# Kernel optimization log

Measured on AMD Instinct MI355X. Metric: run time of the kernel, lower is better.

The kernel has to match this reference:

```python
import jax, jax.numpy as jnp
import numpy as np
from math import factorial

# ----- hyperparams (mirror init_kwargs) -----
HIDDEN = [(32,0,1),(32,0,-1),(8,1,1),(8,1,-1),(4,2,1),(4,2,-1)]  # (mul, l, parity)
SCALAR = [(32,0,1)]
SH_IRR = [(1,0,1),(1,1,-1),(1,2,1)]  # spherical harmonics 0e+1o+2e
EMB, NUM_RBF, R_MAX, MLP_DIM, D_IN = 32, 16, 10.0, 256, 64
N_NODES, N_EDGES, N_GRAPHS = 2048, 8192, 8
EDGE_FEATS_DIM = NUM_RBF + 2*EMB

def _slices(irs):
    s, o = [], 0
    for m, l, _ in irs:
        s.append(o); o += m*(2*l+1)
    return s

def _su2_cg(j1, j2, j3, m1, m2, m3):
    if m1 + m2 != m3:
        return 0.0
    f = factorial
    pref = ((2*j3+1)*f(j3+j1-j2)*f(j3-j1+j2)*f(j1+j2-j3)/f(j1+j2+j3+1))**0.5
    pref *= (f(j3+m3)*f(j3-m3)*f(j1-m1)*f(j1+m1)*f(j2-m2)*f(j2+m2))**0.5
    s = 0.0
    for k in range(0, j1+j2-j3+1):
        if j1-m1-k < 0 or j2+m2-k < 0 or j3-j2+m1+k < 0 or j3-j1-m2+k < 0:
            continue
        s += (-1.0)**k/(f(k)*f(j1+j2-j3-k)*f(j1-m1-k)*f(j2+m2-k)*f(j3-j2+m1+k)*f(j3-j1-m2+k))
    return pref*s

def _q(l):  # real -> complex change of basis (e3nn convention incl. (-i)^l phase)
    q = np.zeros((2*l+1, 2*l+1), dtype=np.complex128)
    for m in range(-l, 0):
        q[l+m, l+abs(m)] = 2**-0.5
        q[l+m, l-abs(m)] = -1j*2**-0.5
    q[l, l] = 1.0
    for m in range(1, l+1):
        q[l+m, l+abs(m)] = (-1)**m*2**-0.5
        q[l+m, l-abs(m)] = 1j*(-1)**m*2**-0.5
    return (-1j)**l*q

def _real_cg(l1, l2, l3):  # real-basis Clebsch-Gordan, unit Frobenius norm (wigner-3j-like)
    C = np.zeros((2*l1+1, 2*l2+1, 2*l3+1), dtype=np.complex128)
    for m1 in range(-l1, l1+1):
        for m2 in range(-l2, l2+1):
            m3 = m1 + m2
            if abs(m3) <= l3:
                C[l1+m1, l2+m2, l3+m3] = _su2_cg(l1, l2, l3, m1, m2, m3)
    w = np.einsum('ai,bj,ck,abc->ijk', _q(l1), _q(l2), np.conj(_q(l3)), C)
    re, im = np.real(w), np.imag(w)
    w = re if np.linalg.norm(re) >= np.linalg.norm(im) else im
    return (w/np.linalg.norm(w)).astype(np.float32)

_CG = {}
def cg(l1, l2, l3):
    if (l1, l2, l3) not in _CG:
        _CG[(l1, l2, l3)] = jnp.asarray(_real_cg(l1, l2, l3))
    return _CG[(l1, l2, l3)]

def _build_layer(ir_in, ir_out):  # FullyConnectedTensorProduct path enumeration
    si = _slices(ir_in)
    paths, woff, fan = [], 0, [0]*len(ir_out)
    for i1, (m1, l1, p1) in enumerate(ir_in):
        for (_, l2, p2) in SH_IRR:
            for i3, (m3, l3, p3) in enumerate(ir_out):
                if p1*p2 == p3 and abs(l1-l2) <= l3 <= l1+l2:
                    paths.append((si[i1], m1, l1, l2, i3, m3, l3, woff))
                    fan[i3] += m1
                    woff += m1*m3
    return paths, woff, fan, ir_out

L_SPECS = [_build_layer(SCALAR, HIDDEN), _build_layer(HIDDEN, HIDDEN),
           _build_layer(HIDDEN, HIDDEN), _build_layer(HIDDEN, SCALAR)]
W_NUMELS = [s[1] for s in L_SPECS]  # [1408, 4320, 4320, 1408]

def spherical_harmonics(u):  # component-normalized real SH, l=0,1,2, on unit vectors
    xc, yc, zc = u[:, 0], u[:, 1], u[:, 2]
    s3, s15, s5 = 3**0.5, 15**0.5, 5**0.5
    return jnp.stack([jnp.ones_like(xc),
                      s3*yc, s3*zc, s3*xc,
                      s15*xc*yc, s15*yc*zc, s5*0.5*(3*zc*zc-1.0), s15*xc*zc,
                      s15*0.5*(xc*xc-yc*yc)], axis=1)

def tp_messages(x, sh, w, spec):  # per-edge equivariant tensor product with edge-dep weights
    paths, _, fan, ir_out = spec
    E = x.shape[0]
    outs = [jnp.zeros((E, m*(2*l+1)), x.dtype) for m, l, _ in ir_out]
    for (o1, m1, l1, l2, i3, m3, l3, woff) in paths:
        xp = x[:, o1:o1+m1*(2*l1+1)].reshape(E, m1, 2*l1+1)
        shp = sh[:, l2*l2:(l2+1)*(l2+1)]
        wp = w[:, woff:woff+m1*m3].reshape(E, m1, m3)
        alpha = float(np.sqrt((2*l3+1)/fan[i3]))  # component/element path normalization
        y = alpha*jnp.einsum('eui,ej,euv,ijk->evk', xp, shp, wp, cg(l1, l2, l3))
        outs[i3] = outs[i3] + y.reshape(E, -1)
    return jnp.concatenate(outs, axis=1)

def batch_norm(h, ir_out, eps=1e-5):  # e3nn-style equivariant batch norm (train stats, identity affine)
    outs, o = [], 0
    for m, l, _ in ir_out:
        d = m*(2*l+1)
        f = h[:, o:o+d].reshape(-1, m, 2*l+1); o += d
        if l == 0:
            f = f - f.mean(axis=0, keepdims=True)
        norm2 = (f*f).mean(axis=(0, 2), keepdims=True)
        outs.append((f*jax.lax.rsqrt(norm2+eps)).reshape(h.shape[0], -1))
    return jnp.concatenate(outs, axis=1)

def scatter_mean(msg, idx, n):
    s = jax.ops.segment_sum(msg, idx, num_segments=n)
    c = jax.ops.segment_sum(jnp.ones((idx.shape[0], 1), msg.dtype), idx, num_segments=n)
    return s/jnp.maximum(c, 1.0)

def _forward(x, pos, edge_index, batch, emb_w, emb_b, layer_params):
    ei = jnp.concatenate([edge_index, edge_index[::-1]], axis=1)  # to_undirected (both directions)
    src, dst = ei[0], ei[1]
    h = x@emb_w + emb_b  # (N, 32)
    vec = pos[src] - pos[dst]
    lengths = jnp.linalg.norm(vec, axis=-1)
    sh = spherical_harmonics(vec/lengths[:, None])  # (E, 9)
    mu = jnp.linspace(0.0, R_MAX, NUM_RBF)
    sigma = R_MAX/NUM_RBF
    rbf = jnp.exp(-(((lengths[:, None]-mu)/sigma)**2))  # (E, 16)
    for li, (w1, b1, w2, b2) in enumerate(layer_params):
        ef = jnp.concatenate([rbf, h[src, :EMB], h[dst, :EMB]], axis=1)  # (E, 80)
        w = jax.nn.relu(ef@w1 + b1)@w2 + b2  # per-edge TP weights (dropout=eval noop)
        upd = scatter_mean(tp_messages(h[dst], sh, w, L_SPECS[li]), src, N_NODES)
        upd = batch_norm(upd, L_SPECS[li][3])
        d = upd.shape[-1]
        h_res = h[:, :d] if h.shape[-1] >= d else jnp.pad(h, ((0, 0), (0, d-h.shape[-1])))
        h = upd + h_res  # residual with pad/truncate (F.pad semantics)
    graph = jax.ops.segment_sum(h, batch, num_segments=N_GRAPHS)
    return h, graph

def setup_inputs():
    key = jax.random.key(0)
    ks = jax.random.split(key, 32)
    inp = {}
    inp['x'] = jax.random.normal(ks[0], (N_NODES, D_IN), jnp.float32)
    inp['pos'] = 3.0*jax.random.normal(ks[1], (N_NODES, 3), jnp.float32)
    s = jax.random.randint(ks[2], (N_EDGES,), 0, N_NODES)
    d = (s + jax.random.randint(ks[3], (N_EDGES,), 1, N_NODES)) % N_NODES  # no self-loops
    inp['edge_index'] = jnp.stack([s, d]).astype(jnp.int32)
    inp['batch'] = jnp.sort(jax.random.randint(ks[4], (N_NODES,), 0, N_GRAPHS)).astype(jnp.int32)
    inp['emb_w'] = jax.random.normal(ks[5], (D_IN, EMB), jnp.float32)/np.sqrt(D_IN)
    inp['emb_b'] = jnp.zeros((EMB,), jnp.float32)
    k = 6
    for i, wn in enumerate(W_NUMELS):
        inp[f'l{i}_w1'] = jax.random.normal(ks[k], (EDGE_FEATS_DIM, MLP_DIM), jnp.float32)/np.sqrt(EDGE_FEATS_DIM); k += 1
        inp[f'l{i}_b1'] = jnp.zeros((MLP_DIM,), jnp.float32)
        inp[f'l{i}_w2'] = jax.random.normal(ks[k], (MLP_DIM, wn), jnp.float32)/np.sqrt(MLP_DIM); k += 1
        inp[f'l{i}_b2'] = jnp.zeros((wn,), jnp.float32)
    return inp

def reference(x, pos, edge_index, batch, emb_w, emb_b,
              l0_w1, l0_b1, l0_w2, l0_b2, l1_w1, l1_b1, l1_w2, l1_b2,
              l2_w1, l2_b1, l2_w2, l2_b2, l3_w1, l3_b1, l3_w2, l3_b2):
    lp = [(l0_w1, l0_b1, l0_w2, l0_b2), (l1_w1, l1_b1, l1_w2, l1_b2),
          (l2_w1, l2_b1, l2_w2, l2_b2), (l3_w1, l3_b1, l3_w2, l3_b2)]
    return _forward(x, pos, edge_index, batch, emb_w, emb_b, lp)
```

## Files before the change

### kernel.cpp

```cpp
#include <hip/hip_runtime.h>
#include <hip/hip_bf16.h>
#include <math.h>

#define NNODES 2048
#define NEDG   8192
#define E2     16384
#define NGRAPH 8
#define HSTR   152

static const int LD_DIN[4]  = {32,152,152,152};
static const int LD_DOUT[4] = {152,152,152,32};
static const int LD_WN[4]   = {1408,4320,4320,1408};
static const int LD_WNP[4]  = {1408,4352,4352,1408};
static const int LD_NCH[4]  = {88,88,88,32};
static const int LD_RES[4]  = {32,152,152,152};
#define WNP_MAX 4352

#define SLOT_MAX    1088
#define CELL_N      20
#define SEG_S_N     164
#define SEG_ENT_MAX 1024

typedef short bf16x8 __attribute__((ext_vector_type(8)));
typedef float f32x4  __attribute__((ext_vector_type(4)));

constexpr double cfact(int n){ double r=1.0; for(int i=2;i<=n;i++) r*=(double)i; return r; }
constexpr double csqrt(double x){
  if(x<=0.0) return 0.0;
  double g = x>1.0? x:1.0;
  for(int i=0;i<64;i++) g=0.5*(g+x/g);
  return g;
}
constexpr double csu2cg(int j1,int j2,int j3,int m1,int m2,int m3){
  if(m1+m2!=m3) return 0.0;
  double pref = csqrt((double)(2*j3+1)*cfact(j3+j1-j2)*cfact(j3-j1+j2)*cfact(j1+j2-j3)/cfact(j1+j2+j3+1));
  pref *= csqrt(cfact(j3+m3)*cfact(j3-m3)*cfact(j1-m1)*cfact(j1+m1)*cfact(j2-m2)*cfact(j2+m2));
  double s=0.0;
  for(int k=0;k<=j1+j2-j3;k++){
    if(j1-m1-k<0||j2+m2-k<0||j3-j2+m1+k<0||j3-j1-m2+k<0) continue;
    double t=1.0/(cfact(k)*cfact(j1+j2-j3-k)*cfact(j1-m1-k)*cfact(j2+m2-k)*cfact(j3-j2+m1+k)*cfact(j3-j1-m2+k));
    s += (k&1)? -t : t;
  }
  return pref*s;
}
struct QM { double r[25]; double i[25]; };
constexpr QM cqmat(int l){
  QM q{};
  const double inv2=0.7071067811865476;
  for(int m=-l;m<0;m++){
    int am=-m;
    q.r[(l+m)*5+(l+am)] = inv2;
    q.i[(l+m)*5+(l-am)] = -inv2;
  }
  q.r[l*5+l]=1.0;
  for(int m=1;m<=l;m++){
    double sgn=(m&1)? -1.0:1.0;
    q.r[(l+m)*5+(l+m)] = sgn*inv2;
    q.i[(l+m)*5+(l-m)] = sgn*inv2;
  }
  for(int rep=0;rep<l;rep++){
    for(int t=0;t<25;t++){ double a=q.r[t], b=q.i[t]; q.r[t]=b; q.i[t]=-a; }
  }
  return q;
}
struct CGCell { float v[125]; };
constexpr CGCell mkcell(int l1,int l2,int l3){
  CGCell out{};
  int lo = l1>l2? l1-l2 : l2-l1;
  if(l3<lo || l3>l1+l2) return out;
  QM q1=cqmat(l1), q2=cqmat(l2), q3=cqmat(l3);
  int n1=2*l1+1,n2=2*l2+1,n3=2*l3+1;
  double C[125]={};
  for(int a=0;a<n1;a++)for(int b=0;b<n2;b++)for(int c=0;c<n3;c++)
    C[a*25+b*5+c]=csu2cg(l1,l2,l3,a-l1,b-l2,c-l3);
  double wr[125]={}, wi[125]={};
  for(int i=0;i<n1;i++)for(int j=0;j<n2;j++)for(int k=0;k<n3;k++){
    double ar=0.0, ai=0.0;
    for(int a=0;a<n1;a++)for(int b=0;b<n2;b++){
      double p1r=q1.r[a*5+i], p1i=q1.i[a*5+i];
      double p2r=q2.r[b*5+j], p2i=q2.i[b*5+j];
      double pr=p1r*p2r-p1i*p2i, pi=p1r*p2i+p1i*p2r;
      for(int c=0;c<n3;c++){
        double cv=C[a*25+b*5+c]; if(cv==0.0) continue;
        double p3r=q3.r[c*5+k], p3i=-q3.i[c*5+k];
        ar += (pr*p3r-pi*p3i)*cv;
        ai += (pr*p3i+pi*p3r)*cv;
      }
    }
    wr[i*25+j*5+k]=ar; wi[i*25+j*5+k]=ai;
  }
  double sr=0.0, si=0.0;
  for(int t=0;t<125;t++){ sr+=wr[t]*wr[t]; si+=wi[t]*wi[t]; }
  double nr=csqrt(sr), ni=csqrt(si);
  bool use_re = nr>=ni;
  double nn = use_re? nr:ni;
  double inv = (nn>1e-300)? 1.0/nn : 0.0;
  for(int t=0;t<125;t++) out.v[t]=(float)((use_re? wr[t]:wi[t])*inv);
  return out;
}
constexpr CGCell CGc0 =mkcell(0,0,0), CGc1 =mkcell(0,0,1), CGc2 =mkcell(0,0,2);
constexpr CGCell CGc3 =mkcell(0,1,0), CGc4 =mkcell(0,1,1), CGc5 =mkcell(0,1,2);
constexpr CGCell CGc6 =mkcell(0,2,0), CGc7 =mkcell(0,2,1), CGc8 =mkcell(0,2,2);
constexpr CGCell CGc9 =mkcell(1,0,0), CGc10=mkcell(1,0,1), CGc11=mkcell(1,0,2);
constexpr CGCell CGc12=mkcell(1,1,0), CGc13=mkcell(1,1,1), CGc14=mkcell(1,1,2);
constexpr CGCell CGc15=mkcell(1,2,0), CGc16=mkcell(1,2,1), CGc17=mkcell(1,2,2);
constexpr CGCell CGc18=mkcell(2,0,0), CGc19=mkcell(2,0,1), CGc20=mkcell(2,0,2);
constexpr CGCell CGc21=mkcell(2,1,0), CGc22=mkcell(2,1,1), CGc23=mkcell(2,1,2);
constexpr CGCell CGc24=mkcell(2,2,0), CGc25=mkcell(2,2,1), CGc26=mkcell(2,2,2);
__constant__ CGCell g_cg[27] = {
  CGc0,CGc1,CGc2,CGc3,CGc4,CGc5,CGc6,CGc7,CGc8,
  CGc9,CGc10,CGc11,CGc12,CGc13,CGc14,CGc15,CGc16,CGc17,
  CGc18,CGc19,CGc20,CGc21,CGc22,CGc23,CGc24,CGc25,CGc26};

#define MAXP 32
struct LayerSpec {
  int np, zc, wn, nc;
  int x_off[MAXP], m1[MAXP], d1[MAXP], sh_off[MAXP], d2[MAXP], d3[MAXP],
      m3[MAXP], woff[MAXP], out_sl[MAXP], cg_idx[MAXP], zbase[MAXP], cell[MAXP];
  float alpha[MAXP];
  int cellcg[16];
};
constexpr LayerSpec mkspec(int li){
  LayerSpec S{};
  const int IRH[6][3]={{32,0,1},{32,0,-1},{8,1,1},{8,1,-1},{4,2,1},{4,2,-1}};
  const int IRS[1][3]={{32,0,1}};
  const int SH2[3][2]={{0,1},{1,-1},{2,1}};
  const int (*irin)[3]  = (li==0)? IRS: IRH; int nin =(li==0)?1:6;
  const int (*irout)[3] = (li==3)? IRS: IRH; int nout=(li==3)?1:6;
  int si_in[6]={}, si_out[6]={};
  { int o=0; for(int i=0;i<nin;i++){ si_in[i]=o;  o+=irin[i][0]*(2*irin[i][1]+1);} }
  { int o=0; for(int i=0;i<nout;i++){ si_out[i]=o; o+=irout[i][0]*(2*irout[i][1]+1);} }
  int fan[6]={};
  int i3a[MAXP]={};
  int np=0, woff=0, zb=0, nc=0;
  for(int i1=0;i1<nin;i1++){
    int m1=irin[i1][0], l1=irin[i1][1], p1=irin[i1][2];
    for(int s=0;s<3;s++){
      int l2=SH2[s][0], p2=SH2[s][1];
      for(int i3=0;i3<nout;i3++){
        int m3=irout[i3][0], l3=irout[i3][1], p3=irout[i3][2];
        int lo = l1>l2? l1-l2 : l2-l1;
        if(p1*p2==p3 && l3>=lo && l3<=l1+l2){
          S.x_off[np]=si_in[i1]; S.m1[np]=m1; S.d1[np]=2*l1+1;
          S.sh_off[np]=l2*l2; S.d2[np]=2*l2+1; S.d3[np]=2*l3+1;
          S.m3[np]=m3; S.woff[np]=woff; S.out_sl[np]=si_out[i3];
          S.cg_idx[np]=l1*9+l2*3+l3; S.zbase[np]=zb;
          int ci=-1;
          for(int c=0;c<nc;c++) if(S.cellcg[c]==S.cg_idx[np]) ci=c;
          if(ci<0){ S.cellcg[nc]=S.cg_idx[np]; ci=nc++; }
          S.cell[np]=ci; i3a[np]=i3;
          np++;
          fan[i3]+=m1; woff+=m1*m3; zb+=m1*(2*l3+1);
        }
      }
    }
  }
  for(int p=0;p<np;p++)
    S.alpha[p]=(float)csqrt((double)(2*((S.d3[p]-1)/2)+1)/(double)fan[i3a[p]]);
  S.np=np; S.zc=zb; S.wn=woff; S.nc=nc;
  return S;
}
constexpr LayerSpec LS0=mkspec(0), LS1=mkspec(1), LS2=mkspec(2), LS3=mkspec(3);
__constant__ LayerSpec g_spec[4]={LS0,LS1,LS2,LS3};

__global__ __launch_bounds__(256) void build_tables_kernel(
    unsigned* __restrict__ slot_tab, unsigned* __restrict__ cell_tab,
    int* __restrict__ seg_start, unsigned* __restrict__ seg_ent,
    int* __restrict__ perm, float* __restrict__ alpha_col){
  __shared__ int vals[256];
  __shared__ int part[256];
  int tid=threadIdx.x;
  int li=blockIdx.x;
  const LayerSpec& S=g_spec[li];
  int np=S.np, zc=S.zc, nc=S.nc, wn=S.wn;
  for(int c=tid;c<nc;c+=256){
    int cgi=S.cellcg[c];
    int l2=(cgi/3)%3;
    cell_tab[li*CELL_N+c]=(unsigned)cgi | ((unsigned)(l2*l2)<<8) | ((unsigned)(2*l2+1)<<12);
  }
  for(int s=tid;s<zc;s+=256){
    int p=0; while(p+1<np && S.zbase[p+1]<=s) p++;
    int rel=s-S.zbase[p];
    int k=rel/S.m1[p], u=rel-k*S.m1[p];
    slot_tab[li*SLOT_MAX+s]=(unsigned)(S.x_off[p]+u*S.d1[p]) | ((unsigned)k<<9) | ((unsigned)S.cell[p]<<12);
  }
  int* pm=perm+li*WNP_MAX;
  float* ac=alpha_col+li*WNP_MAX;
  for(int j=tid;j<wn;j+=256){
    int p=0; while(p+1<np && S.woff[p+1]<=j) p++;
    int rel=j-S.woff[p];
    int v=rel/S.m1[p], u=rel%S.m1[p];
    pm[j]=S.woff[p]+u*S.m3[p]+v;
    ac[j]=S.alpha[p];
  }
  int Dout=(li==3)?32:152;
  for(int d=tid;d<Dout;d+=256){
    int cnt=0;
    for(int p=0;p<np;p++){
      int rel=d-S.out_sl[p];
      if(rel>=0 && rel<S.m3[p]*S.d3[p]) cnt++;
    }
    vals[d]=cnt;
  }
  __syncthreads();
  int v0=(tid<Dout)? vals[tid]:0;
  part[tid]=v0;
  __syncthreads();
  for(int ofs=1;ofs<256;ofs<<=1){
    int v=(tid>=ofs)? part[tid-ofs]:0;
    __syncthreads();
    part[tid]+=v;
    __syncthreads();
  }
  int* sst=seg_start+li*SEG_S_N;
  if(tid<Dout) sst[tid]=part[tid]-v0;
  if(tid==0) sst[Dout]=part[255];
  __syncthreads();
  unsigned* se=seg_ent+li*SEG_ENT_MAX;
  for(int d=tid;d<Dout;d+=256){
    int pos=sst[d];
    for(int p=0;p<np;p++){
      int rel=d-S.out_sl[p];
      if(rel>=0 && rel<S.m3[p]*S.d3[p]){
        int v=rel/S.d3[p], k=rel%S.d3[p];
        unsigned z0=(unsigned)(S.zbase[p]+k*S.m1[p]);
        unsigned w0=(unsigned)(S.woff[p]+v*S.m1[p]);
        unsigned code=(S.m1[p]==32)?2u:((S.m1[p]==8)?1u:0u);
        se[pos]= z0 | (w0<<11) | (code<<24);
        pos++;
      }
    }
  }
}

__global__ void geom_kernel(const float* __restrict__ pos, const int* __restrict__ ei,
                            int* __restrict__ src2, int* __restrict__ dst2,
                            float* __restrict__ sh, float* __restrict__ rbf,
                            int* __restrict__ counts){
  int e=blockIdx.x*256+threadIdx.x;
  if(e>=E2) return;
  int s,d;
  if(e<NEDG){ s=ei[e]; d=ei[NEDG+e]; }
  else { int j=e-NEDG; s=ei[NEDG+j]; d=ei[j]; }
  src2[e]=s; dst2[e]=d;
  atomicAdd(&counts[s],1);
  float vx=pos[s*3+0]-pos[d*3+0];
  float vy=pos[s*3+1]-pos[d*3+1];
  float vz=pos[s*3+2]-pos[d*3+2];
  float len=sqrtf(vx*vx+vy*vy+vz*vz);
  float inv=1.f/len;
  float x=vx*inv, y=vy*inv, z=vz*inv;
  const float s3=1.7320508075688772f, s15=3.872983346207417f, s5=2.23606797749979f;
  float* shp=sh+(size_t)e*9;
  shp[0]=1.f; shp[1]=s3*y; shp[2]=s3*z; shp[3]=s3*x;
  shp[4]=s15*x*y; shp[5]=s15*y*z; shp[6]=s5*0.5f*(3.f*z*z-1.f);
  shp[7]=s15*x*z; shp[8]=s15*0.5f*(x*x-y*y);
  float* rp=rbf+(size_t)e*16;
  const float invsig=1.6f;
  for(int k=0;k<16;k++){
    float t=(len-(10.0f/15.0f)*(float)k)*invsig;
    rp[k]=expf(-t*t);
  }
}

__global__ void scan_kernel(const int* __restrict__ counts, int* __restrict__ row_ptr){
  __shared__ int part[256];
  int t=threadIdx.x;
  int base=t*8;
  int loc[8]; int s=0;
  #pragma unroll
  for(int i=0;i<8;i++){ loc[i]=counts[base+i]; s+=loc[i]; }
  part[t]=s; __syncthreads();
  for(int ofs=1; ofs<256; ofs<<=1){
    int v=(t>=ofs)? part[t-ofs]:0;
    __syncthreads();
    part[t]+=v;
    __syncthreads();
  }
  int run=part[t]-s;
  #pragma unroll
  for(int i=0;i<8;i++){ row_ptr[base+i]=run; run+=loc[i]; }
  if(t==255) row_ptr[NNODES]=run;
}

__global__ void csr_fill_kernel(const int* __restrict__ src2, const int* __restrict__ row_ptr,
                                int* __restrict__ cursor, int* __restrict__ eidx){
  int e=blockIdx.x*256+threadIdx.x;
  if(e>=E2) return;
  int s=src2[e];
  int p=atomicAdd(&cursor[s],1);
  eidx[row_ptr[s]+p]=e;
}

__global__ void embed_kernel(const float* __restrict__ x, const float* __restrict__ W,
                             const float* __restrict__ b, float* __restrict__ h){
  int idx=blockIdx.x*256+threadIdx.x;
  int n=idx>>5, j=idx&31;
  float acc=b[j];
  for(int k=0;k<64;k++) acc += x[n*64+k]*W[k*32+j];
  h[(size_t)n*HSTR+j]=acc;
}

__global__ void cast_w2t_kernel(const float* __restrict__ w2, const int* __restrict__ perm,
                                const float* __restrict__ alpha_col,
                                __hip_bfloat16* __restrict__ w2t, int wn, int wn_pad){
  int idx=blockIdx.x*256+threadIdx.x;
  if(idx>=wn_pad*256) return;
  int j=idx>>8, k=idx&255;
  float v=(j<wn)? w2[(size_t)k*wn+perm[j]]*alpha_col[j] : 0.f;
  w2t[idx]=__float2bfloat16(v);
}

__global__ __launch_bounds__(256) void mlp1_kernel(
    const float* __restrict__ h, const float* __restrict__ rbf,
    const int* __restrict__ src2, const int* __restrict__ dst2,
    const float* __restrict__ w1, const float* __restrict__ b1,
    __hip_bfloat16* __restrict__ hidden, int e_start){
  __shared__ float ef[16][80];
  int tid=threadIdx.x;
  int e0=e_start+blockIdx.x*16;
  for(int t=tid;t<16*80;t+=256){
    int el=t/80, k=t-el*80; int ge=e0+el;
    float v;
    if(k<16)      v=rbf[(size_t)ge*16+k];
    else if(k<48) v=h[(size_t)src2[ge]*HSTR+(k-16)];
    else          v=h[(size_t)dst2[ge]*HSTR+(k-48)];
    ef[el][k]=v;
  }
  __syncthreads();
  float acc[16];
  float bv=b1[tid];
  #pragma unroll
  for(int e=0;e<16;e++) acc[e]=bv;
  for(int k=0;k<80;k++){
    float wv=w1[k*256+tid];
    #pragma unroll
    for(int e=0;e<16;e++) acc[e]+=ef[e][k]*wv;
  }
  int le0=blockIdx.x*16;
  #pragma unroll
  for(int e=0;e<16;e++)
    hidden[(size_t)(le0+e)*256+tid]=__float2bfloat16(fmaxf(acc[e],0.f));
}

__global__ __launch_bounds__(256) void mlp2_mfma_kernel(
    const __hip_bfloat16* __restrict__ hidden,
    const __hip_bfloat16* __restrict__ w2t,
    const float* __restrict__ b2, const int* __restrict__ perm,
    const float* __restrict__ alpha_col,
    __hip_bfloat16* __restrict__ wbuf, int wn, int wn_pad){
  __shared__ __hip_bfloat16 As[128*32];
  __shared__ __hip_bfloat16 Bs[128*32];
  int tid=threadIdx.x;
  int lane=tid&63;
  int m0=blockIdx.x*128, n0=blockIdx.y*128;
  int mw=((tid>>6)&1)*64, nw=(tid>>7)*64;
  f32x4 acc[4][4];
  #pragma unroll
  for(int i=0;i<4;i++)
    #pragma unroll
    for(int j=0;j<4;j++) acc[i][j]=(f32x4){0.f,0.f,0.f,0.f};

  int i0=tid*8, i1=tid*8+2048;
  int ar0=i0>>5, ac0=i0&31, ar1=i1>>5, ac1=i1&31;
  const int q4=lane>>4, c16=lane&15;

  for(int k0=0;k0<256;k0+=32){
    __syncthreads();
    *(uint4*)&As[ar0*32+ac0] = *(const uint4*)&hidden[(size_t)(m0+ar0)*256 + k0 + ac0];
    *(uint4*)&As[ar1*32+ac1] = *(const uint4*)&hidden[(size_t)(m0+ar1)*256 + k0 + ac1];
    *(uint4*)&Bs[ar0*32+ac0] = *(const uint4*)&w2t[(size_t)(n0+ar0)*256 + k0 + ac0];
    *(uint4*)&Bs[ar1*32+ac1] = *(const uint4*)&w2t[(size_t)(n0+ar1)*256 + k0 + ac1];
    __syncthreads();
    bf16x8 af[4], bfr[4];
    #pragma unroll
    for(int mi=0;mi<4;mi++) af[mi]=*(bf16x8*)&As[(mw+mi*16+c16)*32 + q4*8];
    #pragma unroll
    for(int ni=0;ni<4;ni++) bfr[ni]=*(bf16x8*)&Bs[(nw+ni*16+c16)*32 + q4*8];
    #pragma unroll
    for(int mi=0;mi<4;mi++)
      #pragma unroll
      for(int ni=0;ni<4;ni++)
        acc[mi][ni]=__builtin_amdgcn_mfma_f32_16x16x32_bf16(af[mi],bfr[ni],acc[mi][ni],0,0,0);
  }
  #pragma unroll
  for(int ni=0;ni<4;ni++){
    int col=n0+nw+ni*16+c16;
    float bias=(col<wn)? b2[perm[col]]*alpha_col[col]:0.f;
    #pragma unroll
    for(int mi=0;mi<4;mi++){
      int row=m0+mw+mi*16+q4*4;
      #pragma unroll
      for(int rr=0;rr<4;rr++)
        wbuf[(size_t)(row+rr)*wn_pad+col]=__float2bfloat16(acc[mi][ni][rr]+bias);
    }
  }
}

__device__ inline void wave_sync(){
  __builtin_amdgcn_s_waitcnt(0);
  __builtin_amdgcn_wave_barrier();
}

__device__ inline float dot8l(const float* zp, const __hip_bfloat16* wp){
  f32x4 za=*(const f32x4*)zp;
  f32x4 zb=*(const f32x4*)(zp+4);
  uint4 wv=*(const uint4*)wp;
  const __hip_bfloat16* wl=(const __hip_bfloat16*)&wv;
  float s=0.f;
  #pragma unroll
  for(int t=0;t<4;t++) s+=za[t]*__bfloat162float(wl[t]);
  #pragma unroll
  for(int t=0;t<4;t++) s+=zb[t]*__bfloat162float(wl[4+t]);
  return s;
}
__device__ inline float dot4l(const float* zp, const __hip_bfloat16* wp){
  f32x4 za=*(const f32x4*)zp;
  uint2 wv=*(const uint2*)wp;
  const __hip_bfloat16* wl=(const __hip_bfloat16*)&wv;
  float s=0.f;
  #pragma unroll
  for(int t=0;t<4;t++) s+=za[t]*__bfloat162float(wl[t]);
  return s;
}

__global__ __launch_bounds__(128) void tp5_kernel(
    const float* __restrict__ h, const float* __restrict__ sh,
    const __hip_bfloat16* __restrict__ wbuf, const int* __restrict__ dst2,
    const unsigned* __restrict__ slot_tab, const unsigned* __restrict__ cell_tab,
    const int* __restrict__ seg_start, const unsigned* __restrict__ seg_ent,
    float* __restrict__ msg, int e_start, int Din, int Dout, int wstride,
    int zc, int nc){
  __shared__ float xrow[2][160];
  __shared__ float shs[2][12];
  __shared__ float zsm[2][1088];
  __shared__ float Tw[2][376];
  __shared__ __hip_bfloat16 wlds[2][WNP_MAX];
  int tid=threadIdx.x, w=tid>>6, lane=tid&63;
  int le=blockIdx.x*2+w, ge=e_start+le;
  int dn=dst2[ge];
  const __hip_bfloat16* wrow=wbuf+(size_t)le*wstride;
  for(int t=lane;t<(wstride>>3);t+=64)
    *(uint4*)&wlds[w][t*8] = *(const uint4*)&wrow[(size_t)t*8];
  for(int i=lane;i<Din;i+=64) xrow[w][i]=h[(size_t)dn*HSTR+i];
  for(int i=Din+lane;i<160;i+=64) xrow[w][i]=0.f;
  if(lane<9) shs[w][lane]=sh[(size_t)ge*9+lane];
  wave_sync();
  float* T=&Tw[w][0];
  for(int t=lane;t<nc*25;t+=64){
    int c=t/25, r=t-c*25, k=r/5, i=r-k*5;
    unsigned cm=cell_tab[c];
    int cgi=cm&255, sho=(cm>>8)&15, d2=(cm>>12)&7;
    const float* cgp=g_cg[cgi].v + i*25 + k;
    float s=0.f;
    for(int j=0;j<d2;j++) s+=cgp[j*5]*shs[w][sho+j];
    T[t]=s;
  }
  wave_sync();
  const float* xr=&xrow[w][0];
  for(int s=lane;s<zc;s+=64){
    unsigned st=slot_tab[s];
    int xb=st&511, k=(st>>9)&7, c=st>>12;
    const float* Tp=&T[c*25+k*5];
    zsm[w][s]=xr[xb]*Tp[0]+xr[xb+1]*Tp[1]+xr[xb+2]*Tp[2]+xr[xb+3]*Tp[3]+xr[xb+4]*Tp[4];
  }
  wave_sync();
  const __hip_bfloat16* wl=&wlds[w][0];
  const float* zbase=&zsm[w][0];
  for(int d=lane;d<Dout;d+=64){
    int s0=seg_start[d], s1=seg_start[d+1];
    float acc=0.f;
    for(int s=s0;s<s1;s++){
      unsigned sg=seg_ent[s];
      int z0=sg&2047, w0=(sg>>11)&8191, code=sg>>24;
      const float* zp=zbase+z0;
      const __hip_bfloat16* wp=wl+w0;
      if(code==2){
        #pragma unroll
        for(int t=0;t<4;t++) acc+=dot8l(zp+t*8,wp+t*8);
      } else if(code==1){
        acc+=dot8l(zp,wp);
      } else {
        acc+=dot4l(zp,wp);
      }
    }
    msg[(size_t)ge*Dout+d]=acc;
  }
}

__global__ void aggregate_kernel(const float* __restrict__ msg, const int* __restrict__ row_ptr,
                                 const int* __restrict__ eidx, const int* __restrict__ counts,
                                 float* __restrict__ upd, int Dout){
  int n=blockIdx.x; int lane=threadIdx.x;
  int p0=row_ptr[n], p1=row_ptr[n+1];
  int c=counts[n]; if(c<1) c=1;
  float inv=1.f/(float)c;
  for(int d=lane;d<Dout;d+=64){
    float s=0.f;
    for(int p=p0;p<p1;p++) s+=msg[(size_t)eidx[p]*Dout+d];
    upd[(size_t)n*Dout+d]=s*inv;
  }
}

__device__ inline int hidden_chan_of_dim(int d){
  if(d<64)  return d;
  if(d<88)  return 64+(d-64)/3;
  if(d<112) return 72+(d-88)/3;
  if(d<132) return 80+(d-112)/5;
  return 84+(d-132)/5;
}
__device__ inline void hidden_chan_params(int c, int& off, int& dk, int& l0){
  if(c<64){ off=c; dk=1; l0=1; }
  else if(c<72){ off=64+(c-64)*3; dk=3; l0=0; }
  else if(c<80){ off=88+(c-72)*3; dk=3; l0=0; }
  else if(c<84){ off=112+(c-80)*5; dk=5; l0=0; }
  else { off=132+(c-84)*5; dk=5; l0=0; }
}

__global__ void stats_kernel(const float* __restrict__ upd, float* __restrict__ stats,
                             int Dout, int scalar_out){
  int c=blockIdx.x, tid=threadIdx.x;
  int off,dk,l0;
  if(scalar_out){ off=c; dk=1; l0=1; }
  else hidden_chan_params(c,off,dk,l0);
  float s=0.f, s2=0.f;
  int total=NNODES*dk;
  for(int t=tid;t<total;t+=256){
    int n=t/dk, k=t-n*dk;
    float v=upd[(size_t)n*Dout+off+k];
    s+=v; s2+=v*v;
  }
  __shared__ float rs[256], rs2[256];
  rs[tid]=s; rs2[tid]=s2; __syncthreads();
  for(int o=128;o>0;o>>=1){
    if(tid<o){ rs[tid]+=rs[tid+o]; rs2[tid]+=rs2[tid+o]; }
    __syncthreads();
  }
  if(tid==0){
    float cnt=(float)total;
    float mean = l0? rs[0]/cnt : 0.f;
    float var = rs2[0]/cnt - mean*mean;
    stats[c*2]=mean;
    stats[c*2+1]=1.0f/sqrtf(var+1e-5f);
  }
}

__global__ void apply_kernel(const float* __restrict__ upd, const float* __restrict__ stats,
                             const float* __restrict__ h_cur, float* __restrict__ h_next,
                             int Dout, int res_dim, int scalar_out, int out_stride){
  int idx=blockIdx.x*256+threadIdx.x;
  if(idx>=NNODES*Dout) return;
  int n=idx/Dout, d=idx-n*Dout;
  int c = scalar_out? d : hidden_chan_of_dim(d);
  float v=(upd[idx]-stats[2*c])*stats[2*c+1];
  float res=(d<res_dim)? h_cur[(size_t)n*HSTR+d] : 0.f;
  h_next[(size_t)n*out_stride+d]=v+res;
}

__global__ void graph_kernel(const float* __restrict__ hfin, const int* __restrict__ batch,
                             float* __restrict__ gout){
  int idx=blockIdx.x*256+threadIdx.x;
  int n=idx>>5, d=idx&31;
  atomicAdd(&gout[batch[n]*32+d], hfin[idx]);
}

extern "C" void kernel_launch(void* const* d_in, const int* in_sizes, int n_in,
                              void* d_out, int out_size, void* d_ws, size_t ws_size,
                              hipStream_t stream){
  (void)in_sizes; (void)n_in; (void)out_size;
  const float* x    =(const float*)d_in[0];
  const float* pos  =(const float*)d_in[1];
  const int*   ei   =(const int*)d_in[2];
  const int*   batch=(const int*)d_in[3];
  const float* emb_w=(const float*)d_in[4];
  const float* emb_b=(const float*)d_in[5];
  const float *W1[4], *B1[4], *W2[4], *B2[4];
  for(int l=0;l<4;l++){
    W1[l]=(const float*)d_in[6+4*l];
    B1[l]=(const float*)d_in[7+4*l];
    W2[l]=(const float*)d_in[8+4*l];
    B2[l]=(const float*)d_in[9+4*l];
  }
  int ZC[4]={LS0.zc,LS1.zc,LS2.zc,LS3.zc};
  int NC[4]={LS0.nc,LS1.nc,LS2.nc,LS3.nc};

  char* base=(char*)d_ws;
  size_t off=0;
  auto alloc=[&](size_t bytes)->char*{
    off=(off+255)&~(size_t)255;
    char* p=base+off; off+=bytes; return p;
  };
  float*  h_a   =(float*)alloc((size_t)NNODES*HSTR*4);
  float*  h_b   =(float*)alloc((size_t)NNODES*HSTR*4);
  float*  shb   =(float*)alloc((size_t)E2*9*4);
  float*  rbfb  =(float*)alloc((size_t)E2*16*4);
  int*    src2  =(int*)  alloc((size_t)E2*4);
  int*    dst2  =(int*)  alloc((size_t)E2*4);
  int*    counts=(int*)  alloc((size_t)NNODES*4);
  int*    cursor=(int*)  alloc((size_t)NNODES*4);
  int*    row_ptr=(int*) alloc((size_t)(NNODES+4)*4);
  int*    eidx  =(int*)  alloc((size_t)E2*4);
  float*  msg   =(float*)alloc((size_t)E2*HSTR*4);
  float*  upd   =(float*)alloc((size_t)NNODES*HSTR*4);
  float*  stats =(float*)alloc(256*4);
  unsigned* slot_tab=(unsigned*)alloc((size_t)4*SLOT_MAX*4);
  unsigned* cell_tg =(unsigned*)alloc((size_t)4*CELL_N*4);
  int*      seg_s   =(int*)     alloc((size_t)4*SEG_S_N*4);
  unsigned* seg_e   =(unsigned*)alloc((size_t)4*SEG_ENT_MAX*4);
  int*      perm    =(int*)     alloc((size_t)4*WNP_MAX*4);
  float*    alpha_c =(float*)   alloc((size_t)4*WNP_MAX*4);
  __hip_bfloat16* w2t[4];
  for(int l=0;l<4;l++) w2t[l]=(__hip_bfloat16*)alloc((size_t)LD_WNP[l]*256*2);

  int E_CHUNK=E2;
  while(E_CHUNK>128){
    size_t need=off;
    need=(need+255)&~(size_t)255; need+=(size_t)E_CHUNK*256*2;
    need=(need+255)&~(size_t)255; need+=(size_t)E_CHUNK*WNP_MAX*2;
    if(need<=ws_size) break;
    E_CHUNK>>=1;
  }
  __hip_bfloat16* hidden=(__hip_bfloat16*)alloc((size_t)E_CHUNK*256*2);
  __hip_bfloat16* wbuf  =(__hip_bfloat16*)alloc((size_t)E_CHUNK*WNP_MAX*2);

  hipMemsetAsync(counts,0,(size_t)NNODES*4,stream);
  hipMemsetAsync(cursor,0,(size_t)NNODES*4,stream);
  build_tables_kernel<<<4,256,0,stream>>>(slot_tab,cell_tg,seg_s,seg_e,perm,alpha_c);
  geom_kernel<<<E2/256,256,0,stream>>>(pos,ei,src2,dst2,shb,rbfb,counts);
  scan_kernel<<<1,256,0,stream>>>(counts,row_ptr);
  csr_fill_kernel<<<E2/256,256,0,stream>>>(src2,row_ptr,cursor,eidx);
  embed_kernel<<<(NNODES*32)/256,256,0,stream>>>(x,emb_w,emb_b,h_a);
  for(int l=0;l<4;l++)
    cast_w2t_kernel<<<(LD_WNP[l]*256+255)/256,256,0,stream>>>(
        W2[l],perm+l*WNP_MAX,alpha_c+l*WNP_MAX,w2t[l],LD_WN[l],LD_WNP[l]);

  float* h_cur=h_a; float* h_nxt=h_b;
  for(int li=0;li<4;li++){
    int wn=LD_WN[li], wnp=LD_WNP[li], Din=LD_DIN[li], Dout=LD_DOUT[li];
    for(int e0=0;e0<E2;e0+=E_CHUNK){
      mlp1_kernel<<<E_CHUNK/16,256,0,stream>>>(h_cur,rbfb,src2,dst2,W1[li],B1[li],hidden,e0);
      dim3 g2(E_CHUNK/128, wnp/128);
      mlp2_mfma_kernel<<<g2,256,0,stream>>>(hidden,w2t[li],B2[li],perm+li*WNP_MAX,
                                            alpha_c+li*WNP_MAX,wbuf,wn,wnp);
      tp5_kernel<<<E_CHUNK/2,128,0,stream>>>(h_cur,shb,wbuf,dst2,
          slot_tab+li*SLOT_MAX, cell_tg+li*CELL_N,
          seg_s+li*SEG_S_N, seg_e+li*SEG_ENT_MAX,
          msg,e0,Din,Dout,wnp, ZC[li], NC[li]);
    }
    aggregate_kernel<<<NNODES,64,0,stream>>>(msg,row_ptr,eidx,counts,upd,Dout);
    stats_kernel<<<LD_NCH[li],256,0,stream>>>(upd,stats,Dout,li==3?1:0);
    int tot=NNODES*Dout;
    if(li<3)
      apply_kernel<<<(tot+255)/256,256,0,stream>>>(upd,stats,h_cur,h_nxt,Dout,LD_RES[li],0,HSTR);
    else
      apply_kernel<<<(tot+255)/256,256,0,stream>>>(upd,stats,h_cur,(float*)d_out,Dout,LD_RES[li],1,32);
    float* tmp=h_cur; h_cur=h_nxt; h_nxt=tmp;
  }

  float* gout=(float*)d_out + (size_t)NNODES*32;
  hipMemsetAsync(gout,0,(size_t)NGRAPH*32*4,stream);
  graph_kernel<<<(NNODES*32)/256,256,0,stream>>>((const float*)d_out,batch,gout);
}
```

Before: 895.3 us.

## Read per-edge TP weights directly from global memory and interleave output segments

The tensor-product kernel no longer stages each edge's weight row into LDS and instead reads bf16 weights straight from global memory inside the segment dot products. It also packs four edges per 256-thread block instead of two, and each lane now handles up to three output channels in one interleaved loop rather than a strided outer loop. The aim is to cut LDS footprint, raising occupancy, and to remove the staging copy and its barrier. The cost is uncoalesced, scattered global loads of weights, and extra predicated work when the three channels have different segment counts.

```diff
diff --git a/kernel.cpp b/kernel.cpp
--- a/kernel.cpp
+++ b/kernel.cpp
@@ -402,46 +402,56 @@
   __builtin_amdgcn_wave_barrier();
 }
 
-__device__ inline float dot8l(const float* zp, const __hip_bfloat16* wp){
-  f32x4 za=*(const f32x4*)zp;
-  f32x4 zb=*(const f32x4*)(zp+4);
-  uint4 wv=*(const uint4*)wp;
-  const __hip_bfloat16* wl=(const __hip_bfloat16*)&wv;
+__device__ inline float seg_dot(unsigned sg, const float* zbase, const __hip_bfloat16* wrow){
+  int z0=sg&2047, w0=(sg>>11)&8191, code=sg>>24;
+  const float* zp=zbase+z0;
+  const __hip_bfloat16* wp=wrow+w0;
   float s=0.f;
-  #pragma unroll
-  for(int t=0;t<4;t++) s+=za[t]*__bfloat162float(wl[t]);
-  #pragma unroll
-  for(int t=0;t<4;t++) s+=zb[t]*__bfloat162float(wl[4+t]);
+  if(code==2){
+    #pragma unroll
+    for(int t=0;t<4;t++){
+      f32x4 za=*(const f32x4*)(zp+t*8);
+      f32x4 zb=*(const f32x4*)(zp+t*8+4);
+      uint4 wv=*(const uint4*)(wp+t*8);
+      const __hip_bfloat16* wl=(const __hip_bfloat16*)&wv;
+      #pragma unroll
+      for(int q=0;q<4;q++) s+=za[q]*__bfloat162float(wl[q]);
+      #pragma unroll
+      for(int q=0;q<4;q++) s+=zb[q]*__bfloat162float(wl[4+q]);
+    }
+  } else if(code==1){
+    f32x4 za=*(const f32x4*)zp;
+    f32x4 zb=*(const f32x4*)(zp+4);
+    uint4 wv=*(const uint4*)wp;
+    const __hip_bfloat16* wl=(const __hip_bfloat16*)&wv;
+    #pragma unroll
+    for(int q=0;q<4;q++) s+=za[q]*__bfloat162float(wl[q]);
+    #pragma unroll
+    for(int q=0;q<4;q++) s+=zb[q]*__bfloat162float(wl[4+q]);
+  } else {
+    f32x4 za=*(const f32x4*)zp;
+    uint2 wv=*(const uint2*)wp;
+    const __hip_bfloat16* wl=(const __hip_bfloat16*)&wv;
+    #pragma unroll
+    for(int q=0;q<4;q++) s+=za[q]*__bfloat162float(wl[q]);
+  }
   return s;
 }
-__device__ inline float dot4l(const float* zp, const __hip_bfloat16* wp){
-  f32x4 za=*(const f32x4*)zp;
-  uint2 wv=*(const uint2*)wp;
-  const __hip_bfloat16* wl=(const __hip_bfloat16*)&wv;
-  float s=0.f;
-  #pragma unroll
-  for(int t=0;t<4;t++) s+=za[t]*__bfloat162float(wl[t]);
-  return s;
-}
-
-__global__ __launch_bounds__(128) void tp5_kernel(
+
+__global__ __launch_bounds__(256) void tp6_kernel(
     const float* __restrict__ h, const float* __restrict__ sh,
     const __hip_bfloat16* __restrict__ wbuf, const int* __restrict__ dst2,
     const unsigned* __restrict__ slot_tab, const unsigned* __restrict__ cell_tab,
     const int* __restrict__ seg_start, const unsigned* __restrict__ seg_ent,
     float* __restrict__ msg, int e_start, int Din, int Dout, int wstride,
     int zc, int nc){
-  __shared__ float xrow[2][160];
-  __shared__ float shs[2][12];
-  __shared__ float zsm[2][1088];
-  __shared__ float Tw[2][376];
-  __shared__ __hip_bfloat16 wlds[2][WNP_MAX];
+  __shared__ float xrow[4][160];
+  __shared__ float shs[4][12];
+  __shared__ float zsm[4][1088];
+  __shared__ float Tw[4][376];
   int tid=threadIdx.x, w=tid>>6, lane=tid&63;
-  int le=blockIdx.x*2+w, ge=e_start+le;
+  int le=blockIdx.x*4+w, ge=e_start+le;
   int dn=dst2[ge];
-  const __hip_bfloat16* wrow=wbuf+(size_t)le*wstride;
-  for(int t=lane;t<(wstride>>3);t+=64)
-    *(uint4*)&wlds[w][t*8] = *(const uint4*)&wrow[(size_t)t*8];
   for(int i=lane;i<Din;i+=64) xrow[w][i]=h[(size_t)dn*HSTR+i];
   for(int i=Din+lane;i<160;i+=64) xrow[w][i]=0.f;
   if(lane<9) shs[w][lane]=sh[(size_t)ge*9+lane];
@@ -465,27 +475,24 @@
     zsm[w][s]=xr[xb]*Tp[0]+xr[xb+1]*Tp[1]+xr[xb+2]*Tp[2]+xr[xb+3]*Tp[3]+xr[xb+4]*Tp[4];
   }
   wave_sync();
-  const __hip_bfloat16* wl=&wlds[w][0];
+  const __hip_bfloat16* wrow=wbuf+(size_t)le*wstride;
   const float* zbase=&zsm[w][0];
-  for(int d=lane;d<Dout;d+=64){
-    int s0=seg_start[d], s1=seg_start[d+1];
-    float acc=0.f;
-    for(int s=s0;s<s1;s++){
-      unsigned sg=seg_ent[s];
-      int z0=sg&2047, w0=(sg>>11)&8191, code=sg>>24;
-      const float* zp=zbase+z0;
-      const __hip_bfloat16* wp=wl+w0;
-      if(code==2){
-        #pragma unroll
-        for(int t=0;t<4;t++) acc+=dot8l(zp+t*8,wp+t*8);
-      } else if(code==1){
-        acc+=dot8l(zp,wp);
-      } else {
-        acc+=dot4l(zp,wp);
-      }
-    }
-    msg[(size_t)ge*Dout+d]=acc;
-  }
+  int d0=lane, d1=lane+64, d2v=lane+128;
+  bool h2=(d2v<Dout);
+  int p0=seg_start[d0],  q0=seg_start[d0+1];
+  int p1=(d1<Dout)? seg_start[d1]:0, q1=(d1<Dout)? seg_start[d1+1]:0;
+  int p2=h2? seg_start[d2v]:0, q2=h2? seg_start[d2v+1]:0;
+  float a0=0.f, a1=0.f, a2=0.f;
+  int n0=q0-p0, n1=q1-p1, n2=q2-p2;
+  int nmx=n0>n1? n0:n1; if(n2>nmx) nmx=n2;
+  for(int i=0;i<nmx;i++){
+    if(i<n0) a0+=seg_dot(seg_ent[p0+i], zbase, wrow);
+    if(i<n1) a1+=seg_dot(seg_ent[p1+i], zbase, wrow);
+    if(i<n2) a2+=seg_dot(seg_ent[p2+i], zbase, wrow);
+  }
+  if(d0<Dout) msg[(size_t)ge*Dout+d0]=a0;
+  if(d1<Dout) msg[(size_t)ge*Dout+d1]=a1;
+  if(h2)      msg[(size_t)ge*Dout+d2v]=a2;
 }
 
 __global__ void aggregate_kernel(const float* __restrict__ msg, const int* __restrict__ row_ptr,
@@ -642,7 +649,7 @@
       dim3 g2(E_CHUNK/128, wnp/128);
       mlp2_mfma_kernel<<<g2,256,0,stream>>>(hidden,w2t[li],B2[li],perm+li*WNP_MAX,
                                             alpha_c+li*WNP_MAX,wbuf,wn,wnp);
-      tp5_kernel<<<E_CHUNK/2,128,0,stream>>>(h_cur,shb,wbuf,dst2,
+      tp6_kernel<<<E_CHUNK/4,256,0,stream>>>(h_cur,shb,wbuf,dst2,
           slot_tab+li*SLOT_MAX, cell_tg+li*CELL_N,
           seg_s+li*SEG_S_N, seg_e+li*SEG_ENT_MAX,
           msg,e0,Din,Dout,wnp, ZC[li], NC[li]);
```

Result: faster. 863.2 us (-3.6%).
